# Performance work log

Hardware: AMD Instinct MI355X
Metric: run time of the kernel (lower is better)

## Reference

```python
import jax, jax.numpy as jnp
import numpy as np

D_MODEL = 2048
N_HEADS = 16
HEAD_DIM = D_MODEL // N_HEADS  # 128
MAX_POS = 2048


def _precompute_cos_sin(max_pos, head_dim):
    inv_freq = 1.0 / (10000.0 ** (jnp.arange(0, head_dim, 2, dtype=jnp.float32) / head_dim))
    t = jnp.arange(max_pos, dtype=jnp.float32)
    freqs = jnp.outer(t, inv_freq)          # [max_pos, head_dim//2]
    emb = jnp.concatenate([freqs, freqs], axis=-1)  # [max_pos, head_dim]
    return jnp.cos(emb), jnp.sin(emb)


def _rotate_half(x):
    x1, x2 = x[..., : x.shape[-1] // 2], x[..., x.shape[-1] // 2 :]
    return jnp.concatenate([-x2, x1], axis=-1)


def setup_inputs() -> dict:
    key = jax.random.key(0)
    kx, kq, kk, kv, ko = jax.random.split(key, 5)
    B, S = 2, 2048
    x = jax.random.normal(kx, (B, S, D_MODEL), dtype=jnp.float32)
    scale = 1.0 / np.sqrt(D_MODEL)
    # torch Linear weights are [out_features, in_features]
    Wq = jax.random.normal(kq, (D_MODEL, D_MODEL), dtype=jnp.float32) * scale
    Wk = jax.random.normal(kk, (D_MODEL, D_MODEL), dtype=jnp.float32) * scale
    Wv = jax.random.normal(kv, (D_MODEL, D_MODEL), dtype=jnp.float32) * scale
    Wo = jax.random.normal(ko, (D_MODEL, D_MODEL), dtype=jnp.float32) * scale
    cos, sin = _precompute_cos_sin(MAX_POS, HEAD_DIM)
    # causal mask: True where attention is disallowed (masked_fill semantics)
    mask = jnp.triu(jnp.ones((S, S), dtype=bool), k=1)
    mask = jnp.broadcast_to(mask[None], (B, S, S))
    return {"x": x, "Wq": Wq, "Wk": Wk, "Wv": Wv, "Wo": Wo,
            "cos": cos, "sin": sin, "mask": mask}


def reference(x, Wq, Wk, Wv, Wo, cos, sin, mask):
    B, S, _ = x.shape
    H, Dh = N_HEADS, HEAD_DIM
    scaling = Dh ** -0.5

    def split_heads(y):  # [B,S,D] -> [B,H,S,Dh]
        return y.reshape(B, S, H, Dh).transpose(0, 2, 1, 3)

    q = split_heads(x @ Wq.T)
    k = split_heads(x @ Wk.T)
    v = split_heads(x @ Wv.T)

    c = cos[:S][None, None]  # [1,1,S,Dh]
    s = sin[:S][None, None]
    q = q * c + _rotate_half(q) * s
    k = k * c + _rotate_half(k) * s

    scores = jnp.einsum("bhqd,bhkd->bhqk", q, k) * scaling
    scores = jnp.where(mask[:, None], -jnp.inf, scores)
    attn = jax.nn.softmax(scores, axis=-1)
    out = jnp.einsum("bhqk,bhkd->bhqd", attn, v)  # [B,H,S,Dh]
    out = out.transpose(0, 2, 1, 3).reshape(B, S, H * Dh)
    return out @ Wo.T
```

## Files before the change

### kernel.cpp

```cpp
#include <hip/hip_runtime.h>

typedef float f32x4 __attribute__((ext_vector_type(4)));
typedef short s16x8 __attribute__((ext_vector_type(8)));
typedef unsigned short u16;
typedef u16 u16x4 __attribute__((ext_vector_type(4)));

#define SEQ 2048
#define BATCH 2
#define NH 16
#define DH 128
#define DM 2048
#define MROWS (BATCH * SEQ)

__device__ constexpr float SCALE2 = 0.12751879523531f;

__device__ __forceinline__ u16 f2bf(float f) {
  unsigned u = __float_as_uint(f);
  u += 0x7fffu + ((u >> 16) & 1u);
  return (u16)(u >> 16);
}
__device__ __forceinline__ float bf2f(u16 b) {
  return __uint_as_float(((unsigned)b) << 16);
}

__device__ __forceinline__ void gld_lds16(const void* g, void* l) {
  __builtin_amdgcn_global_load_lds(
      (const __attribute__((address_space(1))) unsigned int*)g,
      (__attribute__((address_space(3))) unsigned int*)l, 16, 0, 0);
}

__global__ __launch_bounds__(256) void cast_all(const float* __restrict__ x,
                                                const float* __restrict__ Wq,
                                                const float* __restrict__ Wk,
                                                const float* __restrict__ Wv,
                                                const float* __restrict__ Wo,
                                                u16* __restrict__ xb,
                                                u16* __restrict__ Wqkvb,
                                                u16* __restrict__ Wob) {
  long i = (long)blockIdx.x * 256 + threadIdx.x;
  const float* src;
  u16* dst;
  long off;
  if (i < 2097152)      { src = x;  dst = xb;              off = i; }
  else if (i < 3145728) { src = Wq; dst = Wqkvb;           off = i - 2097152; }
  else if (i < 4194304) { src = Wk; dst = Wqkvb + 4194304; off = i - 3145728; }
  else if (i < 5242880) { src = Wv; dst = Wqkvb + 8388608; off = i - 4194304; }
  else                  { src = Wo; dst = Wob;             off = i - 5242880; }
  float4 v = ((const float4*)src)[off];
  u16x4 o;
  o[0] = f2bf(v.x); o[1] = f2bf(v.y); o[2] = f2bf(v.z); o[3] = f2bf(v.w);
  ((u16x4*)dst)[off] = o;
}


#define GEMM_V3_BODY(A, B)                                                    \
  __shared__ u16 SMEM[49152];                                      \
  u16 (*Alds)[16384] = (u16(*)[16384])SMEM;                    \
  u16 (*Blds)[8192]  = (u16(*)[8192])(SMEM + 32768);           \
  const int tid = threadIdx.x, wave = tid >> 6, lane = tid & 63;              \
  const int r = lane & 15, g = lane >> 4;                                     \
  const int wm = wave >> 1, wn = wave & 1;                                    \
  const int bid = blockIdx.x;                                                 \
  const int swz = (bid & 7) * (gridDim.x >> 3) + (bid >> 3);                  \
  const int m0 = (swz & 15) * 256;                                            \
  const int n0 = (swz >> 4) * 128;                                            \
  const int lrow = lane >> 3;                                                 \
  const int csrc = (lane & 7) ^ lrow;                                         \
  f32x4 acc[4][4] = {};                                                       \
  s16x8 aF[2][4], bF[2][4];                                                   \
  STAGE_A(0, 0, 0); STAGE_B(0, 0, 0); STAGE_A(0, 1, 0); STAGE_B(0, 1, 0);     \
  STAGE_A(1, 0, 1); STAGE_B(1, 0, 1);                                         \
  asm volatile("s_waitcnt vmcnt(3)" ::: "memory");                            \
  __builtin_amdgcn_s_barrier();                                               \
  for (int t = 0; t < 32; ++t) {                                              \
    const int bt = t & 1, bn = bt ^ 1;                                        \
    const u16* Ab = Alds[bt];                                                 \
    const u16* Bb = Blds[bt];                                                 \
    READ_K(0);                                                                \
    __builtin_amdgcn_sched_barrier(0);                                        \
    READ_K(1);                                                                \
    if (t < 31) { STAGE_A(t + 1, 1, bn); STAGE_B(t + 1, 1, bn); }             \
    asm volatile("s_waitcnt lgkmcnt(8)" ::: "memory");                        \
    __builtin_amdgcn_sched_barrier(0);                                        \
    MFMA_K(0);                                                                \
    asm volatile("s_waitcnt lgkmcnt(0)" ::: "memory");                        \
    __builtin_amdgcn_sched_barrier(0);                                        \
    __builtin_amdgcn_s_barrier();                                             \
    if (t < 30) { STAGE_A(t + 2, 0, bt); STAGE_B(t + 2, 0, bt); }             \
    MFMA_K(1);                                                                \
    if (t < 30)       asm volatile("s_waitcnt vmcnt(3)" ::: "memory");        \
    else if (t == 30) asm volatile("s_waitcnt vmcnt(0)" ::: "memory");        \
    __builtin_amdgcn_s_barrier();                                             \
  }

#define STAGE_A(TA, MH, BUF) do {                                             \
  _Pragma("unroll") for (int i_ = 0; i_ < 2; ++i_) {                          \
    const int row0_ = (MH) * 128 + i_ * 64 + wave * 8;                        \
    gld_lds16(A + (long)(m0 + row0_ + lrow) * 2048 + (TA) * 64 + csrc * 8,    \
              &Alds[BUF][row0_ * 64]);                                        \
  } } while (0)
#define STAGE_B(TA, NHh, BUF) do {                                            \
    const int row0_ = (NHh) * 64 + wave * 8;                                  \
    gld_lds16(B + (long)(n0 + row0_ + lrow) * 2048 + (TA) * 64 + csrc * 8,    \
              &Blds[BUF][row0_ * 64]);                                        \
  } while (0)
#define READ_K(KK) do {                                                       \
  _Pragma("unroll") for (int mf = 0; mf < 4; ++mf) {                          \
    const int arow = wm * 64 + mf * 16 + r;                                   \
    aF[KK][mf] = *(const s16x8*)&Ab[arow * 64 +                               \
                                    ((((KK) * 4 + g) ^ (arow & 7)) * 8)];     \
  }                                                                           \
  _Pragma("unroll") for (int nf = 0; nf < 4; ++nf) {                          \
    const int brow = wn * 64 + nf * 16 + r;                                   \
    bF[KK][nf] = *(const s16x8*)&Bb[brow * 64 +                               \
                                    ((((KK) * 4 + g) ^ (brow & 7)) * 8)];     \
  } } while (0)
#define MFMA_K(KK) do {                                                       \
  __builtin_amdgcn_s_setprio(1);                                              \
  _Pragma("unroll") for (int mf = 0; mf < 4; ++mf)                            \
    _Pragma("unroll") for (int nf = 0; nf < 4; ++nf)                          \
      acc[mf][nf] = __builtin_amdgcn_mfma_f32_16x16x32_bf16(                  \
          aF[KK][mf], bF[KK][nf], acc[mf][nf], 0, 0, 0);                      \
  __builtin_amdgcn_s_setprio(0);                                              \
} while (0)

__global__ __launch_bounds__(512, 2) void gemm_qkv8(const u16* __restrict__ A,
                                                    const u16* __restrict__ B,
                                                    const float* __restrict__ cosT,
                                                    const float* __restrict__ sinT,
                                                    u16* __restrict__ Qo,
                                                    u16* __restrict__ Ko,
                                                    u16* __restrict__ Vt) {
  GEMM_V3_BODY(A, B)
  if (n0 < 4096) {
    u16* T = SMEM;
#pragma unroll
    for (int mi = 0; mi < 4; ++mi)
#pragma unroll
      for (int ni = 0; ni < 4; ++ni) {
        const int rl = wm * 64 + mi * 16 + g * 4;
        const int dh = wn * 64 + ni * 16 + r;
#pragma unroll
        for (int q = 0; q < 4; ++q)
          T[(rl + q) * 136 + dh] = f2bf(acc[mi][ni][q]);
      }
    __syncthreads();
    u16* Cb = (n0 < 2048) ? Qo : Ko;
    const int nc0 = n0 & 2047;
    const float sgn = wn ? 1.f : -1.f;
#pragma unroll
    for (int mi = 0; mi < 4; ++mi)
#pragma unroll
      for (int ni = 0; ni < 4; ++ni) {
        const int rl = wm * 64 + mi * 16 + g * 4;
        const int dh = wn * 64 + ni * 16 + r;
#pragma unroll
        for (int q = 0; q < 4; ++q) {
          const int row = m0 + rl + q;
          const int spos = row & 2047;
          const float c  = cosT[spos * 128 + dh];
          const float sn = sinT[spos * 128 + dh];
          const float v = bf2f(T[(rl + q) * 136 + dh]);
          const float p = bf2f(T[(rl + q) * 136 + (dh ^ 64)]);
          Cb[(long)row * 2048 + nc0 + dh] = f2bf(v * c + sgn * p * sn);
        }
      }
  } else {
    u16* T = SMEM;
#pragma unroll
    for (int mi = 0; mi < 4; ++mi)
#pragma unroll
      for (int ni = 0; ni < 4; ++ni) {
        const int d = wn * 64 + ni * 16 + r;
        const int sb = wm * 64 + mi * 16 + g * 4;
        u16x4 w;
#pragma unroll
        for (int q = 0; q < 4; ++q) w[q] = f2bf(acc[mi][ni][q]);
        *(u16x4*)&T[d * 256 + (((sb >> 3) ^ (d & 7)) << 3) + (sb & 7)] = w;
      }
    __syncthreads();
    const int b_ = m0 >> 11, s0l = m0 & 2047;
    const int hh = (n0 - 4096) >> 7;
    const int dd = tid >> 2, part = tid & 3;
    u16* vrow = Vt + ((long)((b_ * 16 + hh) * 128 + dd)) * 2048 + s0l;
#pragma unroll
    for (int cc = 0; cc < 8; ++cc) {
      const int chunk = cc * 4 + part;
      s16x8 v = *(const s16x8*)&T[dd * 256 + ((chunk ^ (dd & 7)) << 3)];
      *(s16x8*)&vrow[chunk * 8] = v;
    }
  }
}

__global__ __launch_bounds__(512, 2) void gemm_wo(const u16* __restrict__ A,
                                                  const u16* __restrict__ B,
                                                  float* __restrict__ C) {
  GEMM_V3_BODY(A, B)
#pragma unroll
  for (int mi = 0; mi < 4; ++mi)
#pragma unroll
    for (int ni = 0; ni < 4; ++ni)
#pragma unroll
      for (int q = 0; q < 4; ++q)
        C[(long)(m0 + wm * 64 + mi * 16 + g * 4 + q) * 2048 +
          n0 + wn * 64 + ni * 16 + r] = acc[mi][ni][q];
}

#undef MFMA_K
#undef READ_K
#undef STAGE_B
#undef STAGE_A
#undef GEMM_V3_BODY


__device__ __forceinline__ void softmax_swapped(
    f32x4 (&s)[4], float& mi, float& li,
    u16 (&pl)[16][64], float (&als)[16],
    int qbase, int k0, int r, int g) {
  const int q = qbase + r;
  const bool edge = (k0 + 63) > qbase;
  float v[16];
#pragma unroll
  for (int kk = 0; kk < 4; kk++)
#pragma unroll
    for (int i = 0; i < 4; i++) {
      float x = s[kk][i] * SCALE2;
      if (edge && (k0 + kk * 16 + g * 4 + i > q)) x = -1e30f;
      v[kk * 4 + i] = x;
    }
  float t8[8], t4[4];
#pragma unroll
  for (int j = 0; j < 8; j++) t8[j] = fmaxf(v[2 * j], v[2 * j + 1]);
#pragma unroll
  for (int j = 0; j < 4; j++) t4[j] = fmaxf(t8[2 * j], t8[2 * j + 1]);
  float mx = fmaxf(fmaxf(t4[0], t4[1]), fmaxf(t4[2], t4[3]));
  mx = fmaxf(mx, __shfl_xor(mx, 16, 64));
  mx = fmaxf(mx, __shfl_xor(mx, 32, 64));
  const float mnew = fmaxf(mi, mx);
  const float a = exp2f(mi - mnew);
  float p[16];
#pragma unroll
  for (int j = 0; j < 16; j++) p[j] = exp2f(v[j] - mnew);
  float s8[8], s4[4];
#pragma unroll
  for (int j = 0; j < 8; j++) s8[j] = p[2 * j] + p[2 * j + 1];
#pragma unroll
  for (int j = 0; j < 4; j++) s4[j] = s8[2 * j] + s8[2 * j + 1];
  float ps = (s4[0] + s4[1]) + (s4[2] + s4[3]);
  ps += __shfl_xor(ps, 16, 64);
  ps += __shfl_xor(ps, 32, 64);
  li = li * a + ps;
  mi = mnew;
  const int sw = (r & 7) << 3;
#pragma unroll
  for (int kk = 0; kk < 4; kk++) {
    u16x4 w;
#pragma unroll
    for (int i = 0; i < 4; i++) w[i] = f2bf(p[kk * 4 + i]);
    *(u16x4*)&pl[r][(kk * 16 + g * 4) ^ sw] = w;
  }
  als[r] = a;
}

__global__ __launch_bounds__(512, 4) void attn_kernel(const u16* __restrict__ Q,
                                                      const u16* __restrict__ K,
                                                      const u16* __restrict__ Vt,
                                                      u16* __restrict__ O) {
  __shared__ u16 Klds[64 * 128];
  __shared__ u16 Vlds[128 * 64];
  __shared__ u16 Plds[8][16][64];
  __shared__ float Alds[8][16];

  const int tid = threadIdx.x, wave = tid >> 6, lane = tid & 63;
  const int r = lane & 15, g = lane >> 4;
  const int bh = blockIdx.x & 31;
  const int jj = blockIdx.x >> 5;
  const int j = (jj < 8) ? jj : 23 - jj;
  const int h = bh & 15, b = bh >> 4;
  const bool isB = wave >= 4;
  const int w4 = wave & 3;
  const int strip = isB ? (31 - j) : j;
  const int q0 = strip * 64 + w4 * 16;
  const int nt = 32 - j;
  const int lastA = j;

  const u16* Qbh = Q + (long)b * SEQ * DM + h * DH;
  const u16* Kbh = K + (long)b * SEQ * DM + h * DH;
  const u16* Vbh = Vt + ((long)(b * NH + h)) * DH * SEQ;

  s16x8 qf[4];
#pragma unroll
  for (int jq = 0; jq < 4; jq++)
    qf[jq] = *(const s16x8*)&Qbh[(long)(q0 + r) * DM + jq * 32 + g * 8];

  f32x4 oacc[8] = {};
  float mi = -1e30f, li = 0.f;

  for (int kt = 0; kt < nt; ++kt) {
    const int k0 = kt * 64;
    __syncthreads();
#pragma unroll
    for (int c = 0; c < 2; ++c) {
      const int s = c * 512 + tid;
      const int krow = s >> 4;
      const int kch = (s & 15) ^ (krow & 7);
      gld_lds16(Kbh + (long)(k0 + krow) * DM + kch * 8,
                &Klds[(c * 512 + wave * 64) * 8]);
      const int vrow = s >> 3;
      const int vch = (s & 7) ^ (vrow & 7);
      gld_lds16(Vbh + (long)vrow * SEQ + k0 + vch * 8,
                &Vlds[(c * 512 + wave * 64) * 8]);
    }
    __syncthreads();

    const bool active = isB || (kt <= lastA);
    if (active) {
      f32x4 sacc[4] = {};
#pragma unroll
      for (int kk = 0; kk < 4; kk++) {
#pragma unroll
        for (int jq = 0; jq < 4; jq++) {
          s16x8 kf = *(const s16x8*)&Klds[(kk * 16 + r) * 128 +
                                          (((jq * 4 + g) ^ (r & 7)) * 8)];
          sacc[kk] = __builtin_amdgcn_mfma_f32_16x16x32_bf16(kf, qf[jq], sacc[kk], 0, 0, 0);
        }
      }
      softmax_swapped(sacc, mi, li, Plds[wave], Alds[wave], q0, k0, r, g);

      f32x4 av = *(const f32x4*)&Alds[wave][g * 4];
#pragma unroll
      for (int f = 0; f < 8; f++)
#pragma unroll
        for (int i = 0; i < 4; i++) oacc[f][i] *= av[i];

      const int sw = (r & 7) << 3;
#pragma unroll
      for (int kc = 0; kc < 2; kc++) {
        s16x8 pf = *(const s16x8*)&Plds[wave][r][(kc * 32 + g * 8) ^ sw];
#pragma unroll
        for (int f = 0; f < 8; f++) {
          s16x8 vf = *(const s16x8*)&Vlds[(f * 16 + r) * 64 +
                                          (((kc * 4 + g) ^ (r & 7)) * 8)];
          oacc[f] = __builtin_amdgcn_mfma_f32_16x16x32_bf16(pf, vf, oacc[f], 0, 0, 0);
        }
      }
    }
  }

  Alds[wave][r] = 1.f / li;
  f32x4 iv = *(const f32x4*)&Alds[wave][g * 4];
  u16* Obh = O + (long)b * SEQ * DM + h * DH;
#pragma unroll
  for (int f = 0; f < 8; f++)
#pragma unroll
    for (int i = 0; i < 4; i++)
      Obh[(long)(q0 + g * 4 + i) * DM + f * 16 + r] = f2bf(oacc[f][i] * iv[i]);
}

extern "C" void kernel_launch(void* const* d_in, const int* in_sizes, int n_in,
                              void* d_out, int out_size, void* d_ws, size_t ws_size,
                              hipStream_t stream) {
  const float* x    = (const float*)d_in[0];
  const float* Wq   = (const float*)d_in[1];
  const float* Wk   = (const float*)d_in[2];
  const float* Wv   = (const float*)d_in[3];
  const float* Wo   = (const float*)d_in[4];
  const float* cosT = (const float*)d_in[5];
  const float* sinT = (const float*)d_in[6];

  if (ws_size < (size_t)134217728) return;

  char* ws = (char*)d_ws;
  u16* xb    = (u16*)(ws);
  u16* Wqkvb = (u16*)(ws + 16777216);
  u16* Wob   = (u16*)(ws + 41943040);
  u16* Qlin  = (u16*)(ws + 50331648);
  u16* Klin  = (u16*)(ws + 67108864);
  u16* Vt    = (u16*)(ws + 100663296);
  u16* Olin  = (u16*)(ws + 117440512);

  cast_all<<<24576, 256, 0, stream>>>(x, Wq, Wk, Wv, Wo, xb, Wqkvb, Wob);

  gemm_qkv8<<<768, 512, 0, stream>>>(xb, Wqkvb, cosT, sinT, Qlin, Klin, Vt);

  attn_kernel<<<512, 512, 0, stream>>>(Qlin, Klin, Vt, Olin);

  gemm_wo<<<256, 512, 0, stream>>>(Olin, Wob, (float*)d_out);
}
```

Measured before the change: 255.4 us.

## Double-buffer K/V tiles in attention and broadcast softmax scales via shuffles

Attention K/V tiles now use two LDS buffers. The next tile's global-to-LDS loads are issued before computing on the current one, and there is one barrier per iteration instead of two. The per-row rescale factor and the final 1/l are broadcast with wave shuffles instead of a round trip through shared memory. This roughly doubles K/V LDS use, which may cut how many blocks fit on a CU.

```diff
diff --git a/kernel.cpp b/kernel.cpp
--- a/kernel.cpp
+++ b/kernel.cpp
@@ -213,10 +213,9 @@
 #undef GEMM_V3_BODY
 
 
-__device__ __forceinline__ void softmax_swapped(
+__device__ __forceinline__ float softmax_swapped(
     f32x4 (&s)[4], float& mi, float& li,
-    u16 (&pl)[16][64], float (&als)[16],
-    int qbase, int k0, int r, int g) {
+    u16 (&pl)[16][64], int qbase, int k0, int r, int g) {
   const int q = qbase + r;
   const bool edge = (k0 + 63) > qbase;
   float v[16];
@@ -259,17 +258,16 @@
     for (int i = 0; i < 4; i++) w[i] = f2bf(p[kk * 4 + i]);
     *(u16x4*)&pl[r][(kk * 16 + g * 4) ^ sw] = w;
   }
-  als[r] = a;
+  return a;
 }
 
 __global__ __launch_bounds__(512, 4) void attn_kernel(const u16* __restrict__ Q,
                                                       const u16* __restrict__ K,
                                                       const u16* __restrict__ Vt,
                                                       u16* __restrict__ O) {
-  __shared__ u16 Klds[64 * 128];
-  __shared__ u16 Vlds[128 * 64];
+  __shared__ u16 Klds[2][64 * 128];
+  __shared__ u16 Vlds[2][128 * 64];
   __shared__ u16 Plds[8][16][64];
-  __shared__ float Alds[8][16];
 
   const int tid = threadIdx.x, wave = tid >> 6, lane = tid & 63;
   const int r = lane & 15, g = lane >> 4;
@@ -296,22 +294,29 @@
   f32x4 oacc[8] = {};
   float mi = -1e30f, li = 0.f;
 
+#define STAGE_KV(KT, BU) do {                                                 \
+  const int k0_ = (KT) * 64;                                                  \
+  _Pragma("unroll") for (int c = 0; c < 2; ++c) {                             \
+    const int s = c * 512 + tid;                                              \
+    const int krow = s >> 4;                                                  \
+    const int kch = (s & 15) ^ (krow & 7);                                    \
+    gld_lds16(Kbh + (long)(k0_ + krow) * DM + kch * 8,                        \
+              &Klds[BU][(c * 512 + wave * 64) * 8]);                          \
+    const int vrow = s >> 3;                                                  \
+    const int vch = (s & 7) ^ (vrow & 7);                                     \
+    gld_lds16(Vbh + (long)vrow * SEQ + k0_ + vch * 8,                         \
+              &Vlds[BU][(c * 512 + wave * 64) * 8]);                          \
+  } } while (0)
+
+  STAGE_KV(0, 0);
+  __syncthreads();
+
   for (int kt = 0; kt < nt; ++kt) {
+    const int bu = kt & 1;
+    if (kt + 1 < nt) STAGE_KV(kt + 1, bu ^ 1);
     const int k0 = kt * 64;
-    __syncthreads();
-#pragma unroll
-    for (int c = 0; c < 2; ++c) {
-      const int s = c * 512 + tid;
-      const int krow = s >> 4;
-      const int kch = (s & 15) ^ (krow & 7);
-      gld_lds16(Kbh + (long)(k0 + krow) * DM + kch * 8,
-                &Klds[(c * 512 + wave * 64) * 8]);
-      const int vrow = s >> 3;
-      const int vch = (s & 7) ^ (vrow & 7);
-      gld_lds16(Vbh + (long)vrow * SEQ + k0 + vch * 8,
-                &Vlds[(c * 512 + wave * 64) * 8]);
-    }
-    __syncthreads();
+    const u16* Kb = Klds[bu];
+    const u16* Vb = Vlds[bu];
 
     const bool active = isB || (kt <= lastA);
     if (active) {
@@ -320,14 +325,15 @@
       for (int kk = 0; kk < 4; kk++) {
 #pragma unroll
         for (int jq = 0; jq < 4; jq++) {
-          s16x8 kf = *(const s16x8*)&Klds[(kk * 16 + r) * 128 +
-                                          (((jq * 4 + g) ^ (r & 7)) * 8)];
+          s16x8 kf = *(const s16x8*)&Kb[(kk * 16 + r) * 128 +
+                                        (((jq * 4 + g) ^ (r & 7)) * 8)];
           sacc[kk] = __builtin_amdgcn_mfma_f32_16x16x32_bf16(kf, qf[jq], sacc[kk], 0, 0, 0);
         }
       }
-      softmax_swapped(sacc, mi, li, Plds[wave], Alds[wave], q0, k0, r, g);
-
-      f32x4 av = *(const f32x4*)&Alds[wave][g * 4];
+      float a = softmax_swapped(sacc, mi, li, Plds[wave], q0, k0, r, g);
+      f32x4 av;
+#pragma unroll
+      for (int i = 0; i < 4; i++) av[i] = __shfl(a, g * 4 + i, 64);
 #pragma unroll
       for (int f = 0; f < 8; f++)
 #pragma unroll
@@ -339,16 +345,20 @@
         s16x8 pf = *(const s16x8*)&Plds[wave][r][(kc * 32 + g * 8) ^ sw];
 #pragma unroll
         for (int f = 0; f < 8; f++) {
-          s16x8 vf = *(const s16x8*)&Vlds[(f * 16 + r) * 64 +
-                                          (((kc * 4 + g) ^ (r & 7)) * 8)];
+          s16x8 vf = *(const s16x8*)&Vb[(f * 16 + r) * 64 +
+                                        (((kc * 4 + g) ^ (r & 7)) * 8)];
           oacc[f] = __builtin_amdgcn_mfma_f32_16x16x32_bf16(pf, vf, oacc[f], 0, 0, 0);
         }
       }
     }
+    __syncthreads();
   }
-
-  Alds[wave][r] = 1.f / li;
-  f32x4 iv = *(const f32x4*)&Alds[wave][g * 4];
+#undef STAGE_KV
+
+  const float inv = 1.f / li;
+  f32x4 iv;
+#pragma unroll
+  for (int i = 0; i < 4; i++) iv[i] = __shfl(inv, g * 4 + i, 64);
   u16* Obh = O + (long)b * SEQ * DM + h * DH;
 #pragma unroll
   for (int f = 0; f < 8; f++)
```

Result: no change. 254.9 us (-0.2%).
